# Kernel tuning notes

Hardware: AMD Instinct MI355X
Metric: run time of the kernel (lower is better)

Reference implementation:

```python
import jax, jax.numpy as jnp
import numpy as np
import math

NUM_HEADS = 12
LAMBDA_INIT = 0.8 - 0.6 * math.exp(-0.3 * (2 - 1))  # lambda_init(depth=2)
SIGMA = 0.5


def _feature_map(t):
    # f(x) = x + 1 if x >= 0 else exp(x)  (ELU+1 style)
    return jnp.where(t >= 0, t + 1.0, jnp.exp(t))


def setup_inputs() -> dict:
    key = jax.random.key(0)
    ks = jax.random.split(key, 9)
    B_, N, C, H = 2048, 64, 384, NUM_HEADS
    d = C // H
    s = 0.02
    return {
        "x": jax.random.normal(ks[0], (B_, N, C), dtype=jnp.float32),
        "qkv_w": jax.random.normal(ks[1], (C, 3 * C), dtype=jnp.float32) * s,
        "qkv_b": jax.random.normal(ks[2], (3 * C,), dtype=jnp.float32) * s,
        "proj_w": jax.random.normal(ks[3], (C, C), dtype=jnp.float32) * s,
        "proj_b": jax.random.normal(ks[4], (C,), dtype=jnp.float32) * s,
        "lambda_k1": jax.random.normal(ks[5], (H, d), dtype=jnp.float32) * 0.1,
        "lambda_v1": jax.random.normal(ks[6], (H, d), dtype=jnp.float32) * 0.1,
        "lambda_k2": jax.random.normal(ks[7], (H, d), dtype=jnp.float32) * 0.1,
        "lambda_v2": jax.random.normal(ks[8], (H, d), dtype=jnp.float32) * 0.1,
    }


def reference(x, qkv_w, qkv_b, proj_w, proj_b,
              lambda_k1, lambda_v1, lambda_k2, lambda_v2):
    B_, N, C = x.shape
    H = NUM_HEADS
    d = C // H
    scale = d ** -0.5

    # qkv projection -> (3, B_, H, N, d)
    qkv = (x @ qkv_w + qkv_b).reshape(B_, N, 3, H, d).transpose(2, 0, 3, 1, 4)
    q, k, v = qkv[0], qkv[1], qkv[2]
    q = q * scale

    # dual-lambda gating: per-head scalar
    lam1 = jnp.exp(jnp.sum(lambda_k1 * lambda_v1, axis=-1))  # (H,)
    lam2 = jnp.exp(jnp.sum(lambda_k2 * lambda_v2, axis=-1))  # (H,)
    lambda_full = lam1 - lam2 + LAMBDA_INIT                   # (H,)

    # feature maps on K^T (B_,H,d,N) and V (B_,H,N,d)
    fk = _feature_map(jnp.swapaxes(k, -1, -2))  # (B_, H, d, N)
    fv = _feature_map(v)                         # (B_, H, N, d)

    # gaussian decay over feature-index pairs (d, d)
    idx = jnp.arange(d, dtype=jnp.float32)
    gauss = jnp.exp(-((idx[:, None] - idx[None, :]) ** 2) / (2.0 * SIGMA ** 2))

    # K^T V products with gaussian decay; key1==key2, value1==value2 in source
    A = jnp.einsum('bhdn,bhne->bhde', fk, fv) * gauss  # (B_, H, d, d)
    attn = A - lambda_full[None, :, None, None] * A

    out = jnp.einsum('bhnd,bhde->bhne', q, attn)       # (B_, H, N, d)
    out = jnp.swapaxes(out, 1, 2).reshape(B_, N, C)
    return out @ proj_w + proj_b
```

## Files before the change

kernel.cpp:

```cpp
#include <hip/hip_runtime.h>
#include <hip/hip_bf16.h>
#include <math.h>


typedef __attribute__((ext_vector_type(8))) short short8;
typedef __attribute__((ext_vector_type(4))) float f32x4;
typedef __attribute__((ext_vector_type(4))) unsigned short us4;

typedef const __attribute__((address_space(1))) unsigned int gu32c;
typedef __attribute__((address_space(3))) unsigned int lu32;

#define MFMA_BF16(A,B,C) __builtin_amdgcn_mfma_f32_16x16x32_bf16(A,B,C,0,0,0)

__device__ __forceinline__ unsigned short f2bf(float f) {
  unsigned int u = __float_as_uint(f);
  u += 0x7FFFu + ((u >> 16) & 1u);
  return (unsigned short)(u >> 16);
}

#define BB 2048
#define NN 64
#define CC 384
#define HH 12
#define DD 32

#define WS_O    0
#define WS_WT   100663296
#define WS_W2T  101548032
#define WS_WB   101842944
#define WS_LAM  101847552

__global__ void setup_kernel(const float* __restrict__ qkv_w,
                             const float* __restrict__ qkv_b,
                             const float* __restrict__ proj_w,
                             const float* __restrict__ lk1, const float* __restrict__ lv1,
                             const float* __restrict__ lk2, const float* __restrict__ lv2,
                             unsigned short* __restrict__ WT,
                             unsigned short* __restrict__ W2T,
                             float* __restrict__ Wb,
                             float* __restrict__ lamS)
{
  const int nWT  = HH * 96 * CC;
  const int nW2T = CC * CC;
  const int nWb  = HH * 96;
  int gid = blockIdx.x * 256 + threadIdx.x;
  if (gid < nWT) {
    int h = gid / (96 * CC);
    int r = gid % (96 * CC);
    int c = r / CC;
    int k = r % CC;
    int col = (c >> 5) * CC + h * DD + (c & 31);
    WT[gid] = f2bf(qkv_w[(size_t)k * (3 * CC) + col]);
  } else if (gid < nWT + nW2T) {
    int j = gid - nWT;
    int n = j / CC, k = j % CC;
    W2T[j] = f2bf(proj_w[(size_t)k * CC + n]);
  } else if (gid < nWT + nW2T + nWb) {
    int j = gid - nWT - nW2T;
    int h = j / 96, c = j % 96;
    Wb[j] = qkv_b[(c >> 5) * CC + h * DD + (c & 31)];
  } else if (gid < nWT + nW2T + nWb + HH) {
    int h = gid - nWT - nW2T - nWb;
    float s1 = 0.f, s2 = 0.f;
    for (int i = 0; i < DD; ++i) {
      s1 += lk1[h * DD + i] * lv1[h * DD + i];
      s2 += lk2[h * DD + i] * lv2[h * DD + i];
    }
    float lambda_init = 0.8f - 0.6f * __expf(-0.3f);
    float lam = __expf(s1) - __expf(s2) + lambda_init;
    lamS[h] = 1.0f - lam;
  }
}

__global__ __launch_bounds__(512, 2) void qkv_attn_kernel(
    const float* __restrict__ x,
    const unsigned short* __restrict__ WT,
    const float* __restrict__ Wb,
    const float* __restrict__ lamS,
    unsigned short* __restrict__ O)
{
  __shared__ __align__(16) char smem[144384];
  unsigned short* Xs       = (unsigned short*)smem;
  unsigned short* WtRegion = (unsigned short*)(smem + 100352);
  unsigned short* Sq       = (unsigned short*)(smem + 124928);
  unsigned short* AtBase   = (unsigned short*)(smem + 139264);

  const int tid  = threadIdx.x;
  const int lane = tid & 63;
  const int wave = tid >> 6;
  const int quad = lane >> 4;
  const int l15  = lane & 15;
  const int rg   = wave >> 1;
  const int ch   = wave & 1;
  const int bb   = wave >> 2;
  const int ww   = wave & 3;

  auto stage_wt = [&](const unsigned short* src0, char* ldsb) {
    {
      int c = tid >> 3, sg = tid & 7;
      const unsigned short* sp = src0 + c * CC + ((sg ^ (c & 7)) << 3);
      __builtin_amdgcn_global_load_lds((gu32c*)(const void*)sp,
          (lu32*)(void*)(ldsb + (tid & ~63) * 16), 16, 0, 0);
    }
    if (tid < 256) {
      int p = 512 + tid;
      int c = p >> 3, sg = p & 7;
      const unsigned short* sp = src0 + c * CC + ((sg ^ (c & 7)) << 3);
      __builtin_amdgcn_global_load_lds((gu32c*)(const void*)sp,
          (lu32*)(void*)(ldsb + 8192 + (tid & ~63) * 16), 16, 0, 0);
    }
  };

  stage_wt(WT, (char*)WtRegion);
  {
    const float* xb = x + (size_t)blockIdx.x * (2 * NN * CC);
    #pragma unroll
    for (int it = 0; it < 24; ++it) {
      int i = it * 512 + tid;
      int row = i / 96, c4 = i % 96;
      float4 v = *(const float4*)(xb + row * CC + c4 * 4);
      ushort4 o;
      o.x = f2bf(v.x); o.y = f2bf(v.y); o.z = f2bf(v.z); o.w = f2bf(v.w);
      *(ushort4*)(Xs + row * 392 + c4 * 4) = o;
    }
  }
  __syncthreads();

  for (int h = 0; h < HH; ++h) {
    const unsigned short* Wh = WT + (size_t)h * (96 * CC);

    f32x4 acc[2][3];
    #pragma unroll
    for (int mt = 0; mt < 2; ++mt)
      #pragma unroll
      for (int t = 0; t < 3; ++t) acc[mt][t] = (f32x4){0.f, 0.f, 0.f, 0.f};

    for (int kc = 0; kc < 6; ++kc) {
      if (kc < 5)
        stage_wt(Wh + (kc + 1) * 64, (char*)WtRegion + ((kc + 1) & 1) * 12288);
      const unsigned short* Wt = WtRegion + (kc & 1) * 6144;
      __builtin_amdgcn_s_setprio(1);
      #pragma unroll
      for (int step = 0; step < 2; ++step) {
        const int kk = step * 32 + quad * 8;
        const int sw = (((step * 4 + quad) ^ (l15 & 7)) << 3);
        short8 a0 = *(const short8*)(Xs + (rg * 32 +      l15) * 392 + kc * 64 + kk);
        short8 a1 = *(const short8*)(Xs + (rg * 32 + 16 + l15) * 392 + kc * 64 + kk);
        #pragma unroll
        for (int t = 0; t < 3; ++t) {
          short8 bfr = *(const short8*)(Wt + (ch * 48 + t * 16 + l15) * 64 + sw);
          acc[0][t] = MFMA_BF16(a0, bfr, acc[0][t]);
          acc[1][t] = MFMA_BF16(a1, bfr, acc[1][t]);
        }
      }
      __builtin_amdgcn_s_setprio(0);
      __syncthreads();
    }

    {
      unsigned short* StK = WtRegion + bb * 4608;
      unsigned short* StV = StK + 2304;
      #pragma unroll
      for (int mt = 0; mt < 2; ++mt) {
        const int rowb = rg * 32 + mt * 16 + quad * 4;
        const int nloc = rowb & 63;
        #pragma unroll
        for (int t = 0; t < 3; ++t) {
          const int c0 = ch * 48 + t * 16;
          const int c  = c0 + l15;
          float bias = Wb[h * 96 + c];
          if (c0 < 32) {
            #pragma unroll
            for (int r = 0; r < 4; ++r) {
              float v = (acc[mt][t][r] + bias) * 0.17677669529663689f;
              Sq[(rowb + r) * 56 + c] = f2bf(v);
            }
          } else {
            us4 pk;
            #pragma unroll
            for (int r = 0; r < 4; ++r) {
              float v = acc[mt][t][r] + bias;
              v = (v >= 0.f) ? (v + 1.f) : __expf(v);
              pk[r] = f2bf(v);
            }
            if (c0 < 64) *(us4*)(StK + (c0 - 32 + l15) * 72 + nloc) = pk;
            else         *(us4*)(StV + (c0 - 64 + l15) * 72 + nloc) = pk;
          }
        }
      }
    }
    __syncthreads();

    {
      const unsigned short* StK = WtRegion + bb * 4608;
      const unsigned short* StV = StK + 2304;
      const int i0 = (ww & 1) * 16;
      const int e0 = (ww >> 1) * 16;
      f32x4 accA = (f32x4){0.f, 0.f, 0.f, 0.f};
      #pragma unroll
      for (int n0 = 0; n0 < 64; n0 += 32) {
        short8 afr = *(const short8*)(StK + (i0 + l15) * 72 + n0 + quad * 8);
        short8 bfr = *(const short8*)(StV + (e0 + l15) * 72 + n0 + quad * 8);
        accA = MFMA_BF16(afr, bfr, accA);
      }
      const float lsc = lamS[h];
      unsigned short* At = AtBase + bb * 1280;
      const int e = e0 + l15;
      us4 pk;
      #pragma unroll
      for (int r = 0; r < 4; ++r) {
        int i = i0 + quad * 4 + r;
        float diff = (float)(i - e);
        pk[r] = f2bf(accA[r] * lsc * __expf(-2.0f * diff * diff));
      }
      *(us4*)(At + e * 40 + i0 + quad * 4) = pk;
    }
    __syncthreads();

    if (h < HH - 1) stage_wt(WT + (size_t)(h + 1) * (96 * CC), (char*)WtRegion);

    {
      const unsigned short* At = AtBase + bb * 1280;
      short8 aq = *(const short8*)(Sq + (wave * 16 + l15) * 56 + quad * 8);
      const size_t bg = (size_t)blockIdx.x * 2 + bb;
      const int nw0 = ww * 16 + quad * 4;
      #pragma unroll
      for (int t2 = 0; t2 < 2; ++t2) {
        short8 bA = *(const short8*)(At + (t2 * 16 + l15) * 40 + quad * 8);
        f32x4 accO = MFMA_BF16(aq, bA, ((f32x4){0.f, 0.f, 0.f, 0.f}));
        #pragma unroll
        for (int r = 0; r < 4; ++r) {
          O[(bg * NN + nw0 + r) * CC + h * DD + t2 * 16 + l15] = f2bf(accO[r]);
        }
      }
    }
    __syncthreads();
  }
}

__global__ __launch_bounds__(256, 2) void proj_kernel(
    const unsigned short* __restrict__ O,
    const unsigned short* __restrict__ W2T,
    const float* __restrict__ proj_b,
    float* __restrict__ out)
{
  __shared__ __align__(16) char smem[65536];

  const int tid  = threadIdx.x;
  const int lane = tid & 63, wave = tid >> 6;
  const int quad = lane >> 4, l15 = lane & 15;
  const int mw = (wave >> 1) * 64, nw = (wave & 1) * 64;

  const int lid = blockIdx.x;
  const int nid = (lid & 7) * 384 + (lid >> 3);
  const int bm = nid / 3, bn = nid % 3;
  const int m0 = bm * 128, n0 = bn * 128;

  auto stg = [&](int kc, int sel) {
    char* ab = smem + sel * 32768;
    #pragma unroll
    for (int i = 0; i < 4; ++i) {
      int p = i * 256 + tid;
      int row = p >> 3, sg = p & 7;
      int sw = ((sg ^ (row & 7)) << 3);
      const unsigned short* sa = O   + (size_t)(m0 + row) * CC + kc * 64 + sw;
      const unsigned short* sb = W2T + (size_t)(n0 + row) * CC + kc * 64 + sw;
      int ub = (p & ~63) * 16;
      __builtin_amdgcn_global_load_lds((gu32c*)(const void*)sa,
          (lu32*)(void*)(ab + ub), 16, 0, 0);
      __builtin_amdgcn_global_load_lds((gu32c*)(const void*)sb,
          (lu32*)(void*)(ab + 16384 + ub), 16, 0, 0);
    }
  };

  f32x4 acc[4][4];
  #pragma unroll
  for (int i = 0; i < 4; ++i)
    #pragma unroll
    for (int j = 0; j < 4; ++j) acc[i][j] = (f32x4){0.f, 0.f, 0.f, 0.f};

  stg(0, 0);
  __syncthreads();
  for (int kc = 0; kc < 6; ++kc) {
    if (kc < 5) stg(kc + 1, (kc + 1) & 1);
    const unsigned short* As = (const unsigned short*)(smem + (kc & 1) * 32768);
    const unsigned short* Bs = As + 8192;
    __builtin_amdgcn_s_setprio(1);
    #pragma unroll
    for (int step = 0; step < 2; ++step) {
      const int sw = (((step * 4 + quad) ^ (l15 & 7)) << 3);
      short8 af[4], bf_[4];
      #pragma unroll
      for (int t = 0; t < 4; ++t) {
        af[t]  = *(const short8*)(As + (mw + t * 16 + l15) * 64 + sw);
        bf_[t] = *(const short8*)(Bs + (nw + t * 16 + l15) * 64 + sw);
      }
      #pragma unroll
      for (int i = 0; i < 4; ++i)
        #pragma unroll
        for (int j = 0; j < 4; ++j)
          acc[i][j] = MFMA_BF16(af[i], bf_[j], acc[i][j]);
    }
    __builtin_amdgcn_s_setprio(0);
    __syncthreads();
  }

  #pragma unroll
  for (int j = 0; j < 4; ++j) {
    int col = n0 + nw + j * 16 + l15;
    float bias = proj_b[col];
    #pragma unroll
    for (int i = 0; i < 4; ++i) {
      int row0 = m0 + mw + i * 16 + quad * 4;
      #pragma unroll
      for (int r = 0; r < 4; ++r) {
        out[(size_t)(row0 + r) * CC + col] = acc[i][j][r] + bias;
      }
    }
  }
}

extern "C" void kernel_launch(void* const* d_in, const int* in_sizes, int n_in,
                              void* d_out, int out_size, void* d_ws, size_t ws_size,
                              hipStream_t stream) {
  const float* x      = (const float*)d_in[0];
  const float* qkv_w  = (const float*)d_in[1];
  const float* qkv_b  = (const float*)d_in[2];
  const float* proj_w = (const float*)d_in[3];
  const float* proj_b = (const float*)d_in[4];
  const float* lk1    = (const float*)d_in[5];
  const float* lv1    = (const float*)d_in[6];
  const float* lk2    = (const float*)d_in[7];
  const float* lv2    = (const float*)d_in[8];

  char* ws = (char*)d_ws;
  unsigned short* O   = (unsigned short*)(ws + WS_O);
  unsigned short* WT  = (unsigned short*)(ws + WS_WT);
  unsigned short* W2T = (unsigned short*)(ws + WS_W2T);
  float* Wb           = (float*)(ws + WS_WB);
  float* lamS         = (float*)(ws + WS_LAM);

  setup_kernel<<<2309, 256, 0, stream>>>(qkv_w, qkv_b, proj_w,
                                         lk1, lv1, lk2, lv2,
                                         WT, W2T, Wb, lamS);
  qkv_attn_kernel<<<1024, 512, 0, stream>>>(x, WT, Wb, lamS, O);
  proj_kernel<<<3072, 256, 0, stream>>>(O, W2T, proj_b, (float*)d_out);
}
```

Before: 622.7 us.

## Fuse output projection into attention kernel and keep X fragments in registers

```diff
diff --git a/kernel.cpp b/kernel.cpp
--- a/kernel.cpp
+++ b/kernel.cpp
@@ -24,11 +24,10 @@
 #define HH 12
 #define DD 32
 
-#define WS_O    0
-#define WS_WT   100663296
-#define WS_W2T  101548032
-#define WS_WB   101842944
-#define WS_LAM  101847552
+#define WS_WT   0
+#define WS_W2T  884736
+#define WS_WB   1179648
+#define WS_LAM  1184256
 
 __global__ void setup_kernel(const float* __restrict__ qkv_w,
                              const float* __restrict__ qkv_b,
@@ -72,15 +71,17 @@
   }
 }
 
-__global__ __launch_bounds__(512, 2) void qkv_attn_kernel(
+__global__ __launch_bounds__(512, 2) void fused_kernel(
     const float* __restrict__ x,
     const unsigned short* __restrict__ WT,
     const float* __restrict__ Wb,
     const float* __restrict__ lamS,
-    unsigned short* __restrict__ O)
+    const unsigned short* __restrict__ W2T,
+    const float* __restrict__ proj_b,
+    float* __restrict__ out)
 {
   __shared__ __align__(16) char smem[144384];
-  unsigned short* Xs       = (unsigned short*)smem;
+  unsigned short* OX       = (unsigned short*)smem;
   unsigned short* WtRegion = (unsigned short*)(smem + 100352);
   unsigned short* Sq       = (unsigned short*)(smem + 124928);
   unsigned short* AtBase   = (unsigned short*)(smem + 139264);
@@ -108,6 +109,25 @@
       const unsigned short* sp = src0 + c * CC + ((sg ^ (c & 7)) << 3);
       __builtin_amdgcn_global_load_lds((gu32c*)(const void*)sp,
           (lu32*)(void*)(ldsb + 8192 + (tid & ~63) * 16), 16, 0, 0);
+    }
+  };
+
+  auto stage_w2 = [&](int nh, int kc, int sel) {
+    char* ldsb = (char*)WtRegion + sel * 12288;
+    {
+      int row = tid >> 2, sg = tid & 3;
+      const unsigned short* sp = W2T + (size_t)(nh * 192 + row) * CC + kc * 32
+                                 + ((sg ^ ((row >> 1) & 3)) << 3);
+      __builtin_amdgcn_global_load_lds((gu32c*)(const void*)sp,
+          (lu32*)(void*)(ldsb + (tid & ~63) * 16), 16, 0, 0);
+    }
+    if (tid < 256) {
+      int p = 512 + tid;
+      int row = p >> 2, sg = p & 3;
+      const unsigned short* sp = W2T + (size_t)(nh * 192 + row) * CC + kc * 32
+                                 + ((sg ^ ((row >> 1) & 3)) << 3);
+      __builtin_amdgcn_global_load_lds((gu32c*)(const void*)sp,
+          (lu32*)(void*)(ldsb + (p & ~63) * 16), 16, 0, 0);
     }
   };
 
@@ -121,10 +141,18 @@
       float4 v = *(const float4*)(xb + row * CC + c4 * 4);
       ushort4 o;
       o.x = f2bf(v.x); o.y = f2bf(v.y); o.z = f2bf(v.z); o.w = f2bf(v.w);
-      *(ushort4*)(Xs + row * 392 + c4 * 4) = o;
+      *(ushort4*)(OX + row * 392 + c4 * 4) = o;
     }
   }
   __syncthreads();
+
+  short8 xa[2][12];
+  #pragma unroll
+  for (int mt = 0; mt < 2; ++mt)
+    #pragma unroll
+    for (int s = 0; s < 12; ++s)
+      xa[mt][s] = *(const short8*)(OX + (rg * 32 + mt * 16 + l15) * 392
+                                   + s * 32 + quad * 8);
 
   for (int h = 0; h < HH; ++h) {
     const unsigned short* Wh = WT + (size_t)h * (96 * CC);
@@ -135,6 +163,7 @@
       #pragma unroll
       for (int t = 0; t < 3; ++t) acc[mt][t] = (f32x4){0.f, 0.f, 0.f, 0.f};
 
+    #pragma unroll
     for (int kc = 0; kc < 6; ++kc) {
       if (kc < 5)
         stage_wt(Wh + (kc + 1) * 64, (char*)WtRegion + ((kc + 1) & 1) * 12288);
@@ -142,15 +171,12 @@
       __builtin_amdgcn_s_setprio(1);
       #pragma unroll
       for (int step = 0; step < 2; ++step) {
-        const int kk = step * 32 + quad * 8;
         const int sw = (((step * 4 + quad) ^ (l15 & 7)) << 3);
-        short8 a0 = *(const short8*)(Xs + (rg * 32 +      l15) * 392 + kc * 64 + kk);
-        short8 a1 = *(const short8*)(Xs + (rg * 32 + 16 + l15) * 392 + kc * 64 + kk);
         #pragma unroll
         for (int t = 0; t < 3; ++t) {
           short8 bfr = *(const short8*)(Wt + (ch * 48 + t * 16 + l15) * 64 + sw);
-          acc[0][t] = MFMA_BF16(a0, bfr, acc[0][t]);
-          acc[1][t] = MFMA_BF16(a1, bfr, acc[1][t]);
+          acc[0][t] = MFMA_BF16(xa[0][kc * 2 + step], bfr, acc[0][t]);
+          acc[1][t] = MFMA_BF16(xa[1][kc * 2 + step], bfr, acc[1][t]);
         }
       }
       __builtin_amdgcn_s_setprio(0);
@@ -218,103 +244,68 @@
     __syncthreads();
 
     if (h < HH - 1) stage_wt(WT + (size_t)(h + 1) * (96 * CC), (char*)WtRegion);
+    else            stage_w2(0, 0, 0);
 
     {
       const unsigned short* At = AtBase + bb * 1280;
       short8 aq = *(const short8*)(Sq + (wave * 16 + l15) * 56 + quad * 8);
-      const size_t bg = (size_t)blockIdx.x * 2 + bb;
-      const int nw0 = ww * 16 + quad * 4;
+      const int lrow = wave * 16 + quad * 4;
       #pragma unroll
       for (int t2 = 0; t2 < 2; ++t2) {
         short8 bA = *(const short8*)(At + (t2 * 16 + l15) * 40 + quad * 8);
         f32x4 accO = MFMA_BF16(aq, bA, ((f32x4){0.f, 0.f, 0.f, 0.f}));
         #pragma unroll
-        for (int r = 0; r < 4; ++r) {
-          O[(bg * NN + nw0 + r) * CC + h * DD + t2 * 16 + l15] = f2bf(accO[r]);
-        }
+        for (int r = 0; r < 4; ++r)
+          OX[(lrow + r) * 392 + h * DD + t2 * 16 + l15] = f2bf(accO[r]);
       }
     }
     __syncthreads();
   }
-}
-
-__global__ __launch_bounds__(256, 2) void proj_kernel(
-    const unsigned short* __restrict__ O,
-    const unsigned short* __restrict__ W2T,
-    const float* __restrict__ proj_b,
-    float* __restrict__ out)
-{
-  __shared__ __align__(16) char smem[65536];
-
-  const int tid  = threadIdx.x;
-  const int lane = tid & 63, wave = tid >> 6;
-  const int quad = lane >> 4, l15 = lane & 15;
-  const int mw = (wave >> 1) * 64, nw = (wave & 1) * 64;
-
-  const int lid = blockIdx.x;
-  const int nid = (lid & 7) * 384 + (lid >> 3);
-  const int bm = nid / 3, bn = nid % 3;
-  const int m0 = bm * 128, n0 = bn * 128;
-
-  auto stg = [&](int kc, int sel) {
-    char* ab = smem + sel * 32768;
-    #pragma unroll
-    for (int i = 0; i < 4; ++i) {
-      int p = i * 256 + tid;
-      int row = p >> 3, sg = p & 7;
-      int sw = ((sg ^ (row & 7)) << 3);
-      const unsigned short* sa = O   + (size_t)(m0 + row) * CC + kc * 64 + sw;
-      const unsigned short* sb = W2T + (size_t)(n0 + row) * CC + kc * 64 + sw;
-      int ub = (p & ~63) * 16;
-      __builtin_amdgcn_global_load_lds((gu32c*)(const void*)sa,
-          (lu32*)(void*)(ab + ub), 16, 0, 0);
-      __builtin_amdgcn_global_load_lds((gu32c*)(const void*)sb,
-          (lu32*)(void*)(ab + 16384 + ub), 16, 0, 0);
-    }
-  };
-
-  f32x4 acc[4][4];
-  #pragma unroll
-  for (int i = 0; i < 4; ++i)
-    #pragma unroll
-    for (int j = 0; j < 4; ++j) acc[i][j] = (f32x4){0.f, 0.f, 0.f, 0.f};
-
-  stg(0, 0);
-  __syncthreads();
-  for (int kc = 0; kc < 6; ++kc) {
-    if (kc < 5) stg(kc + 1, (kc + 1) & 1);
-    const unsigned short* As = (const unsigned short*)(smem + (kc & 1) * 32768);
-    const unsigned short* Bs = As + 8192;
-    __builtin_amdgcn_s_setprio(1);
-    #pragma unroll
-    for (int step = 0; step < 2; ++step) {
-      const int sw = (((step * 4 + quad) ^ (l15 & 7)) << 3);
-      short8 af[4], bf_[4];
-      #pragma unroll
-      for (int t = 0; t < 4; ++t) {
-        af[t]  = *(const short8*)(As + (mw + t * 16 + l15) * 64 + sw);
-        bf_[t] = *(const short8*)(Bs + (nw + t * 16 + l15) * 64 + sw);
-      }
-      #pragma unroll
-      for (int i = 0; i < 4; ++i)
-        #pragma unroll
-        for (int j = 0; j < 4; ++j)
-          acc[i][j] = MFMA_BF16(af[i], bf_[j], acc[i][j]);
-    }
-    __builtin_amdgcn_s_setprio(0);
-    __syncthreads();
-  }
-
-  #pragma unroll
-  for (int j = 0; j < 4; ++j) {
-    int col = n0 + nw + j * 16 + l15;
-    float bias = proj_b[col];
-    #pragma unroll
-    for (int i = 0; i < 4; ++i) {
-      int row0 = m0 + mw + i * 16 + quad * 4;
-      #pragma unroll
-      for (int r = 0; r < 4; ++r) {
-        out[(size_t)(row0 + r) * CC + col] = acc[i][j][r] + bias;
+
+  {
+    const int rg2 = wave >> 1;
+    const int cg2 = wave & 1;
+    const size_t rowg0 = (size_t)blockIdx.x * 128 + rg2 * 32;
+
+    for (int nh = 0; nh < 2; ++nh) {
+      f32x4 acc2[2][6];
+      #pragma unroll
+      for (int mt = 0; mt < 2; ++mt)
+        #pragma unroll
+        for (int t = 0; t < 6; ++t) acc2[mt][t] = (f32x4){0.f, 0.f, 0.f, 0.f};
+
+      for (int kc = 0; kc < 12; ++kc) {
+        if (kc < 11)      stage_w2(nh, kc + 1, (kc + 1) & 1);
+        else if (nh == 0) stage_w2(1, 0, 0);
+        const unsigned short* Wp = WtRegion + (kc & 1) * 6144;
+        __builtin_amdgcn_s_setprio(1);
+        short8 a0 = *(const short8*)(OX + (rg2 * 32 +      l15) * 392
+                                     + kc * 32 + quad * 8);
+        short8 a1 = *(const short8*)(OX + (rg2 * 32 + 16 + l15) * 392
+                                     + kc * 32 + quad * 8);
+        #pragma unroll
+        for (int t = 0; t < 6; ++t) {
+          const int row = cg2 * 96 + t * 16 + l15;
+          short8 b = *(const short8*)(Wp + row * 32
+                                      + ((quad ^ ((row >> 1) & 3)) << 3));
+          acc2[0][t] = MFMA_BF16(a0, b, acc2[0][t]);
+          acc2[1][t] = MFMA_BF16(a1, b, acc2[1][t]);
+        }
+        __builtin_amdgcn_s_setprio(0);
+        __syncthreads();
+      }
+
+      #pragma unroll
+      for (int t = 0; t < 6; ++t) {
+        const int col = nh * 192 + cg2 * 96 + t * 16 + l15;
+        const float bias = proj_b[col];
+        #pragma unroll
+        for (int mt = 0; mt < 2; ++mt) {
+          const size_t row0 = rowg0 + mt * 16 + quad * 4;
+          #pragma unroll
+          for (int r = 0; r < 4; ++r)
+            out[(row0 + r) * CC + col] = acc2[mt][t][r] + bias;
+        }
       }
     }
   }
@@ -334,7 +325,6 @@
   const float* lv2    = (const float*)d_in[8];
 
   char* ws = (char*)d_ws;
-  unsigned short* O   = (unsigned short*)(ws + WS_O);
   unsigned short* WT  = (unsigned short*)(ws + WS_WT);
   unsigned short* W2T = (unsigned short*)(ws + WS_W2T);
   float* Wb           = (float*)(ws + WS_WB);
@@ -343,6 +333,6 @@
   setup_kernel<<<2309, 256, 0, stream>>>(qkv_w, qkv_b, proj_w,
                                          lk1, lv1, lk2, lv2,
                                          WT, W2T, Wb, lamS);
-  qkv_attn_kernel<<<1024, 512, 0, stream>>>(x, WT, Wb, lamS, O);
-  proj_kernel<<<3072, 256, 0, stream>>>(O, W2T, proj_b, (float*)d_out);
+  fused_kernel<<<1024, 512, 0, stream>>>(x, WT, Wb, lamS, W2T, proj_b,
+                                         (float*)d_out);
 }
```

New measurement: 590.7 us. 1.05x faster.
